# Kernel optimization log

Measured on AMD Instinct MI355X. Metric: run time of the kernel, lower is better.

## Reference

```python
import jax, jax.numpy as jnp
import numpy as np

DIM = 64
N_NEIGHBOR = 32
N_ENTITY = 1_000_000
N_RELATION = 64
N_USER = 500_000
BATCH = 16384


def _xavier_uniform(key, shape):
    fan_in, fan_out = shape[0], shape[1]
    bound = float(np.sqrt(6.0 / (fan_in + fan_out)))
    return jax.random.uniform(key, shape, jnp.float32, -bound, bound)


def setup_inputs() -> dict:
    key = jax.random.key(0)
    ks = jax.random.split(key, 10)
    users = jax.random.randint(ks[0], (BATCH,), 0, N_USER)
    items = jax.random.randint(ks[1], (BATCH,), 0, N_ENTITY)
    label = jnp.round(jax.random.uniform(ks[2], (BATCH,), jnp.float32))
    neighbor_rel = jax.random.randint(ks[3], (BATCH, N_NEIGHBOR), 0, N_RELATION)
    neighbor_tail = jax.random.randint(ks[4], (BATCH, N_NEIGHBOR), 0, N_ENTITY)
    user_emb = _xavier_uniform(ks[5], (N_USER, DIM))
    entity_emb = _xavier_uniform(ks[6], (N_ENTITY, DIM))
    relation_emb = _xavier_uniform(ks[7], (N_RELATION, DIM))
    in_dim = 2 * N_NEIGHBOR * DIM
    wb = float(np.sqrt(1.0 / in_dim))  # torch Linear default init bound
    gen_W = jax.random.uniform(ks[8], (DIM, in_dim), jnp.float32, -wb, wb)
    gen_b = jax.random.uniform(ks[9], (DIM,), jnp.float32, -wb, wb)
    return {"users": users, "items": items, "label": label,
            "neighbor_rel": neighbor_rel, "neighbor_tail": neighbor_tail,
            "user_emb": user_emb, "entity_emb": entity_emb,
            "relation_emb": relation_emb, "gen_W": gen_W, "gen_b": gen_b}


def _bce(p, y):
    # torch BCELoss: clamps log terms at -100, mean reduction
    logp = jnp.clip(jnp.log(p), -100.0)
    log1mp = jnp.clip(jnp.log1p(-p), -100.0)
    return -jnp.mean(y * logp + (1.0 - y) * log1mp)


def reference(users, items, label, neighbor_rel, neighbor_tail,
              user_emb, entity_emb, relation_emb, gen_W, gen_b):
    u = user_emb[users]                       # [B, D]
    i = entity_emb[items]                     # [B, D]
    predict = jax.nn.sigmoid(jnp.sum(u * i, axis=1))

    rel = relation_emb[neighbor_rel]          # [B, K, D]
    tail = entity_emb[neighbor_tail]          # [B, K, D]
    t_r = jnp.concatenate([rel, tail], axis=-1).reshape(u.shape[0], -1)  # [B, 2*K*D]
    false_item = jax.nn.sigmoid(t_r @ gen_W.T + gen_b)                   # [B, D]
    false_predict = jax.nn.sigmoid(jnp.sum(u * false_item, axis=1))

    return _bce(predict, label) + _bce(false_predict, label)
```

## Files before the change

kernel.cpp:

```cpp
#include <hip/hip_runtime.h>
#include <hip/hip_bf16.h>

#define BATCH 16384
#define DIM   64
#define NNB   32
#define INDIM 4096
#define BR    64
#define KC    128

typedef __attribute__((ext_vector_type(8))) short          s16x8;
typedef __attribute__((ext_vector_type(4))) float          f32x4;
typedef __attribute__((ext_vector_type(4))) unsigned int   u32x4;
typedef __attribute__((ext_vector_type(4))) unsigned short u16x4;

__device__ __forceinline__ float bf2f(unsigned short u) {
    union { unsigned int i; float f; } v;
    v.i = ((unsigned int)u) << 16;
    return v.f;
}

template<bool FP32>
__device__ __forceinline__ float ldT(const void* p, size_t i) {
    if constexpr (FP32) return ((const float*)p)[i];
    else                return bf2f(((const unsigned short*)p)[i]);
}

__global__ void kgnn_probe(const unsigned int* __restrict__ lab, int* __restrict__ flag) {
    if (threadIdx.x == 0) {
        int ok = 1;
        for (int i = 0; i < 32; ++i) {
            unsigned int w = lab[i];
            if (!(w == 0u || w == 0x3F800000u)) ok = 0;
        }
        *flag = ok;
    }
}

template<bool FP32>
__global__ __launch_bounds__(512, 2) void kgnn_mfma(
    const int* __restrict__ users, const int* __restrict__ items,
    const void* __restrict__ label_, const int* __restrict__ nrel,
    const int* __restrict__ ntail,  const void* __restrict__ uemb_,
    const void* __restrict__ eemb_, const void* __restrict__ remb_,
    const void* __restrict__ W_,    const void* __restrict__ b_,
    double* __restrict__ acc, const int* __restrict__ flag, const int force)
{
    if (force < 0 && *flag != (FP32 ? 1 : 0)) return;

    constexpr int TB = FP32 ? 32768 : 16384;
    constexpr int LO = 16384;
    __shared__ __align__(16) unsigned char ldsA[TB];
    __shared__ __align__(16) unsigned char ldsW[TB];
    __shared__ float p1s[BR];
    __shared__ float p2s[BR][2];

    const int t    = threadIdx.x;
    const int base = blockIdx.x * BR;
    const int lane = t & 63;
    const int w    = t >> 6;
    const int rt   = w & 3;
    const int dh   = w >> 2;
    const int r16  = lane & 15;
    const int kg   = lane >> 4;

    u32x4  rA16[2], rW16[2];
    float4 rA32[4], rW32[4];

    auto LOADS = [&](int n) {
        if constexpr (!FP32) {
            #pragma unroll
            for (int it = 0; it < 2; ++it) {
                const int lid = it * 512 + t;
                const int seg = lid >> 3, ln = lid & 7;
                const int row = seg >> 1, half = seg & 1;
                const int idx = half ? ntail[(size_t)(base + row) * NNB + n]
                                     : nrel [(size_t)(base + row) * NNB + n];
                const unsigned short* tbl = (const unsigned short*)(half ? eemb_ : remb_);
                rA16[it] = *(const u32x4*)(tbl + (size_t)idx * DIM + ln * 8);
            }
            #pragma unroll
            for (int it = 0; it < 2; ++it) {
                const int lid = it * 512 + t;
                const int d = lid >> 4, ln = lid & 15;
                rW16[it] = *(const u32x4*)((const unsigned short*)W_
                              + (size_t)d * INDIM + (size_t)n * KC + ln * 8);
            }
        } else {
            #pragma unroll
            for (int it = 0; it < 4; ++it) {
                const int lid = it * 512 + t;
                const int seg = lid >> 4, ln = lid & 15;
                const int row = seg >> 1, half = seg & 1;
                const int idx = half ? ntail[(size_t)(base + row) * NNB + n]
                                     : nrel [(size_t)(base + row) * NNB + n];
                const float* tbl = (const float*)(half ? eemb_ : remb_);
                rA32[it] = ((const float4*)(tbl + (size_t)idx * DIM))[ln];
            }
            #pragma unroll
            for (int it = 0; it < 4; ++it) {
                const int lid = it * 512 + t;
                const int d = lid >> 5, ln = lid & 31;
                rW32[it] = *(const float4*)((const float*)W_
                              + (size_t)d * INDIM + (size_t)n * KC + ln * 4);
            }
        }
    };

    auto split4 = [](const float4 v, u16x4& h, u16x4& l) {
        const float xs[4] = { v.x, v.y, v.z, v.w };
        #pragma unroll
        for (int j = 0; j < 4; ++j) {
            union { float f; unsigned u; } a, b, c;
            a.f = xs[j];
            const unsigned short hh = (unsigned short)(a.u >> 16);
            b.u = ((unsigned)hh) << 16;
            c.f = xs[j] - b.f;
            h[j] = hh;
            l[j] = (unsigned short)(c.u >> 16);
        }
    };

    auto WRITE = [&]() {
        if constexpr (!FP32) {
            #pragma unroll
            for (int it = 0; it < 2; ++it) {
                const int lid = it * 512 + t;
                const int seg = lid >> 3, ln = lid & 7;
                const int row = seg >> 1, half = seg & 1;
                const int byte = row * 256 + ((half * 128 + ln * 16) ^ ((row & 7) << 4));
                *(u32x4*)&ldsA[byte] = rA16[it];
            }
            #pragma unroll
            for (int it = 0; it < 2; ++it) {
                const int lid = it * 512 + t;
                const int d = lid >> 4, ln = lid & 15;
                const int byte = d * 256 + ((ln * 16) ^ ((d & 7) << 4));
                *(u32x4*)&ldsW[byte] = rW16[it];
            }
        } else {
            #pragma unroll
            for (int it = 0; it < 4; ++it) {
                const int lid = it * 512 + t;
                const int seg = lid >> 4, ln = lid & 15;
                const int row = seg >> 1, half = seg & 1;
                u16x4 h, l; split4(rA32[it], h, l);
                const int byte = row * 256 + ((half * 128 + ln * 8) ^ ((row & 7) << 4));
                *(u16x4*)&ldsA[byte]      = h;
                *(u16x4*)&ldsA[LO + byte] = l;
            }
            #pragma unroll
            for (int it = 0; it < 4; ++it) {
                const int lid = it * 512 + t;
                const int d = lid >> 5, ln = lid & 31;
                u16x4 h, l; split4(rW32[it], h, l);
                const int byte = d * 256 + ((ln * 8) ^ ((d & 7) << 4));
                *(u16x4*)&ldsW[byte]      = h;
                *(u16x4*)&ldsW[LO + byte] = l;
            }
        }
    };

    f32x4 acc0 = {0.f, 0.f, 0.f, 0.f};
    f32x4 acc1 = {0.f, 0.f, 0.f, 0.f};

    LOADS(0);
    WRITE();
    __syncthreads();

    for (int n = 0; n < NNB; ++n) {
        const bool more = (n + 1 < NNB);
        if (more) LOADS(n + 1);

        #pragma unroll
        for (int kk = 0; kk < 4; ++kk) {
            const int cb  = (kk * 64 + kg * 16) ^ ((r16 & 7) << 4);
            const int ra  = (rt * 16 + r16) * 256 + cb;
            const int rb0 = (dh * 32 + r16) * 256 + cb;
            const int rb1 = rb0 + 16 * 256;
            if constexpr (!FP32) {
                const s16x8 a  = *(const s16x8*)&ldsA[ra];
                const s16x8 b0 = *(const s16x8*)&ldsW[rb0];
                const s16x8 b1 = *(const s16x8*)&ldsW[rb1];
                acc0 = __builtin_amdgcn_mfma_f32_16x16x32_bf16(a, b0, acc0, 0, 0, 0);
                acc1 = __builtin_amdgcn_mfma_f32_16x16x32_bf16(a, b1, acc1, 0, 0, 0);
            } else {
                const s16x8 ah  = *(const s16x8*)&ldsA[ra];
                const s16x8 al  = *(const s16x8*)&ldsA[LO + ra];
                const s16x8 bh0 = *(const s16x8*)&ldsW[rb0];
                const s16x8 bl0 = *(const s16x8*)&ldsW[LO + rb0];
                const s16x8 bh1 = *(const s16x8*)&ldsW[rb1];
                const s16x8 bl1 = *(const s16x8*)&ldsW[LO + rb1];
                acc0 = __builtin_amdgcn_mfma_f32_16x16x32_bf16(ah, bh0, acc0, 0, 0, 0);
                acc0 = __builtin_amdgcn_mfma_f32_16x16x32_bf16(ah, bl0, acc0, 0, 0, 0);
                acc0 = __builtin_amdgcn_mfma_f32_16x16x32_bf16(al, bh0, acc0, 0, 0, 0);
                acc1 = __builtin_amdgcn_mfma_f32_16x16x32_bf16(ah, bh1, acc1, 0, 0, 0);
                acc1 = __builtin_amdgcn_mfma_f32_16x16x32_bf16(ah, bl1, acc1, 0, 0, 0);
                acc1 = __builtin_amdgcn_mfma_f32_16x16x32_bf16(al, bh1, acc1, 0, 0, 0);
            }
        }
        __syncthreads();
        if (more) WRITE();
        __syncthreads();
    }

    float part1[4] = {0.f, 0.f, 0.f, 0.f};
    float part2[4] = {0.f, 0.f, 0.f, 0.f};
    #pragma unroll
    for (int q = 0; q < 4; ++q) {
        const int r   = rt * 16 + kg * 4 + q;
        const int row = base + r;
        const int uid = users[row];
        #pragma unroll
        for (int j = 0; j < 2; ++j) {
            const int d  = (dh * 2 + j) * 16 + r16;
            const float fl = (j == 0 ? acc0[q] : acc1[q]) + ldT<FP32>(b_, d);
            const float fi = 1.f / (1.f + expf(-fl));
            const float uv = ldT<FP32>(uemb_, (size_t)uid * DIM + d);
            part2[q] += uv * fi;
        }
        if (dh == 0) {
            const int iid = items[row];
            #pragma unroll
            for (int jj = 0; jj < 4; ++jj) {
                const int d = jj * 16 + r16;
                const float uv = ldT<FP32>(uemb_, (size_t)uid * DIM + d);
                const float iv = ldT<FP32>(eemb_, (size_t)iid * DIM + d);
                part1[q] += uv * iv;
            }
        }
    }
    #pragma unroll
    for (int m = 1; m < 16; m <<= 1) {
        #pragma unroll
        for (int q = 0; q < 4; ++q) {
            part2[q] += __shfl_xor(part2[q], m, 64);
            part1[q] += __shfl_xor(part1[q], m, 64);
        }
    }
    if (r16 == 0) {
        #pragma unroll
        for (int q = 0; q < 4; ++q) {
            const int r = rt * 16 + kg * 4 + q;
            p2s[r][dh] = part2[q];
            if (dh == 0) p1s[r] = part1[q];
        }
    }
    __syncthreads();

    if (t < BR) {
        const int r = t, row = base + r;
        const float p1 = p1s[r];
        const float p2 = p2s[r][0] + p2s[r][1];
        const float y  = ldT<FP32>(label_, row);
        const float pa = 1.f / (1.f + expf(-p1));
        const float pb = 1.f / (1.f + expf(-p2));
        float term =
              y * fmaxf(logf(pa), -100.f) + (1.f - y) * fmaxf(log1pf(-pa), -100.f)
            + y * fmaxf(logf(pb), -100.f) + (1.f - y) * fmaxf(log1pf(-pb), -100.f);
        #pragma unroll
        for (int m = 1; m < 64; m <<= 1) term += __shfl_xor(term, m, 64);
        if (r == 0) atomicAdd(acc, (double)term);
    }
}

__global__ void kgnn_fin(const double* __restrict__ acc,
                         const int* __restrict__ flag, void* __restrict__ out,
                         const int mode) {
    if (threadIdx.x == 0 && blockIdx.x == 0) {
        const int m = (mode < 0) ? *flag : mode;
        const float loss = (float)(-(*acc) / (double)BATCH);
        if (m) ((float*)out)[0] = loss;
        else   ((__hip_bfloat16*)out)[0] = __float2bfloat16(loss);
    }
}

extern "C" void kernel_launch(void* const* d_in, const int* in_sizes, int n_in,
                              void* d_out, int out_size, void* d_ws, size_t ws_size,
                              hipStream_t stream) {
    const int* users = (const int*)d_in[0];
    const int* items = (const int*)d_in[1];
    const void* label = d_in[2];
    const int* nrel  = (const int*)d_in[3];
    const int* ntail = (const int*)d_in[4];
    const void* uemb = d_in[5];
    const void* eemb = d_in[6];
    const void* remb = d_in[7];
    const void* genW = d_in[8];
    const void* genb = d_in[9];

    double* acc = (double*)d_ws;
    int* flag   = (int*)((char*)d_ws + 8);
    hipMemsetAsync(d_ws, 0, 16, stream);

    const bool f32sz  = (out_size == 4) && (in_sizes[5] == 128000000);
    const bool bf16sz = (out_size == 2) && (in_sizes[5] == 64000000);
    const int grid = BATCH / BR;

    if (f32sz) {
        kgnn_mfma<true><<<grid, 512, 0, stream>>>(
            users, items, label, nrel, ntail, uemb, eemb, remb, genW, genb, acc, flag, 1);
        kgnn_fin<<<1, 64, 0, stream>>>(acc, flag, d_out, 1);
    } else if (bf16sz) {
        kgnn_mfma<false><<<grid, 512, 0, stream>>>(
            users, items, label, nrel, ntail, uemb, eemb, remb, genW, genb, acc, flag, 1);
        kgnn_fin<<<1, 64, 0, stream>>>(acc, flag, d_out, 0);
    } else {
        kgnn_probe<<<1, 64, 0, stream>>>((const unsigned int*)label, flag);
        kgnn_mfma<false><<<grid, 512, 0, stream>>>(
            users, items, label, nrel, ntail, uemb, eemb, remb, genW, genb, acc, flag, -1);
        kgnn_mfma<true><<<grid, 512, 0, stream>>>(
            users, items, label, nrel, ntail, uemb, eemb, remb, genW, genb, acc, flag, -1);
        kgnn_fin<<<1, 64, 0, stream>>>(acc, flag, d_out, -1);
    }
}
```

Baseline: 439.8 us.

## Rewrite gather-GEMM to load operands directly into registers with split-K waves

The kernel drops the LDS-staged, double-buffered A/W tiles. Each wave now gathers embedding rows and W slices straight from global memory into MFMA operands, with the neighbor indices cached in LDS. Block rows shrink from 64 to 32, the K dimension is split across two wave groups that are reduced through LDS, occupancy is raised to 4 blocks per CU, and the final reduction writes per-block partial sums instead of using double atomics. This removes the per-step barriers and LDS traffic. In exchange, W is re-read from global or L2 by every block with no LDS reuse, and the fp32 path recomputes the W hi/lo split in every block.

Result: slower. 522.0 us (+18.7%).

```diff
diff --git a/kernel.cpp b/kernel.cpp
--- a/kernel.cpp
+++ b/kernel.cpp
@@ -5,12 +5,11 @@
 #define DIM   64
 #define NNB   32
 #define INDIM 4096
-#define BR    64
-#define KC    128
+#define BR    32
+#define NBLK  (BATCH / BR)
 
 typedef __attribute__((ext_vector_type(8))) short          s16x8;
 typedef __attribute__((ext_vector_type(4))) float          f32x4;
-typedef __attribute__((ext_vector_type(4))) unsigned int   u32x4;
 typedef __attribute__((ext_vector_type(4))) unsigned short u16x4;
 
 __device__ __forceinline__ float bf2f(unsigned short u) {
@@ -23,6 +22,33 @@
 __device__ __forceinline__ float ldT(const void* p, size_t i) {
     if constexpr (FP32) return ((const float*)p)[i];
     else                return bf2f(((const unsigned short*)p)[i]);
+}
+
+template<bool FP32>
+__device__ __forceinline__ f32x4 ld4(const void* p, size_t i) {
+    if constexpr (FP32) {
+        return *(const f32x4*)((const float*)p + i);
+    } else {
+        const u16x4 v = *(const u16x4*)((const unsigned short*)p + i);
+        f32x4 r;
+        #pragma unroll
+        for (int j = 0; j < 4; ++j) r[j] = bf2f(v[j]);
+        return r;
+    }
+}
+
+__device__ __forceinline__ void split8(const f32x4 x, const f32x4 y, s16x8& h, s16x8& l) {
+    #pragma unroll
+    for (int j = 0; j < 8; ++j) {
+        const float v = (j < 4) ? x[j] : y[j - 4];
+        union { float f; unsigned u; } a, b, c;
+        a.f = v;
+        const unsigned short hh = (unsigned short)(a.u >> 16);
+        b.u = ((unsigned)hh) << 16;
+        c.f = v - b.f;
+        h[j] = (short)hh;
+        l[j] = (short)(c.u >> 16);
+    }
 }
 
 __global__ void kgnn_probe(const unsigned int* __restrict__ lab, int* __restrict__ flag) {
@@ -37,240 +63,173 @@
 }
 
 template<bool FP32>
-__global__ __launch_bounds__(512, 2) void kgnn_mfma(
+__global__ __launch_bounds__(512, 4) void kgnn_gemm(
     const int* __restrict__ users, const int* __restrict__ items,
     const void* __restrict__ label_, const int* __restrict__ nrel,
     const int* __restrict__ ntail,  const void* __restrict__ uemb_,
     const void* __restrict__ eemb_, const void* __restrict__ remb_,
     const void* __restrict__ W_,    const void* __restrict__ b_,
-    double* __restrict__ acc, const int* __restrict__ flag, const int force)
+    double* __restrict__ acc, double* __restrict__ bsum,
+    const int* __restrict__ flag, const int force)
 {
     if (force < 0 && *flag != (FP32 ? 1 : 0)) return;
 
-    constexpr int TB = FP32 ? 32768 : 16384;
-    constexpr int LO = 16384;
-    __shared__ __align__(16) unsigned char ldsA[TB];
-    __shared__ __align__(16) unsigned char ldsW[TB];
-    __shared__ float p1s[BR];
-    __shared__ float p2s[BR][2];
+    __shared__ int   sidx[2][BR][NNB + 1];
+    __shared__ float fl[2][BR][DIM];
+    __shared__ float st[BR];
 
     const int t    = threadIdx.x;
     const int base = blockIdx.x * BR;
     const int lane = t & 63;
     const int w    = t >> 6;
-    const int rt   = w & 3;
-    const int dh   = w >> 2;
     const int r16  = lane & 15;
     const int kg   = lane >> 4;
-
-    u32x4  rA16[2], rW16[2];
-    float4 rA32[4], rW32[4];
-
-    auto LOADS = [&](int n) {
-        if constexpr (!FP32) {
+    const int dt   = w & 3;
+    const int kh   = w >> 2;
+
+    #pragma unroll
+    for (int it = 0; it < 2; ++it) {
+        const int e = it * 512 + t;
+        const int row = e >> 5, n = e & 31;
+        sidx[0][row][n] = nrel [(size_t)base * NNB + e];
+        sidx[1][row][n] = ntail[(size_t)base * NNB + e];
+    }
+    __syncthreads();
+
+    f32x4 ac[2] = { {0.f,0.f,0.f,0.f}, {0.f,0.f,0.f,0.f} };
+    const int dcol = dt * 16 + r16;
+
+    if constexpr (!FP32) {
+        const unsigned short* E  = (const unsigned short*)eemb_;
+        const unsigned short* R  = (const unsigned short*)remb_;
+        const unsigned short* wb = (const unsigned short*)W_ + (size_t)dcol * INDIM + kg * 8;
+        #pragma unroll 2
+        for (int nn = 0; nn < NNB / 2; ++nn) {
+            const int n = kh * (NNB / 2) + nn;
+            const unsigned short* wn = wb + n * 128;
+            const s16x8 b0 = *(const s16x8*)(wn);
+            const s16x8 b1 = *(const s16x8*)(wn + 32);
+            const s16x8 b2 = *(const s16x8*)(wn + 64);
+            const s16x8 b3 = *(const s16x8*)(wn + 96);
             #pragma unroll
-            for (int it = 0; it < 2; ++it) {
-                const int lid = it * 512 + t;
-                const int seg = lid >> 3, ln = lid & 7;
-                const int row = seg >> 1, half = seg & 1;
-                const int idx = half ? ntail[(size_t)(base + row) * NNB + n]
-                                     : nrel [(size_t)(base + row) * NNB + n];
-                const unsigned short* tbl = (const unsigned short*)(half ? eemb_ : remb_);
-                rA16[it] = *(const u32x4*)(tbl + (size_t)idx * DIM + ln * 8);
+            for (int rt = 0; rt < 2; ++rt) {
+                const int ri = sidx[0][rt * 16 + r16][n];
+                const int ti = sidx[1][rt * 16 + r16][n];
+                const unsigned short* rr = R + (size_t)ri * DIM + kg * 8;
+                const unsigned short* tr = E + (size_t)ti * DIM + kg * 8;
+                const s16x8 a0 = *(const s16x8*)(rr);
+                const s16x8 a1 = *(const s16x8*)(rr + 32);
+                const s16x8 a2 = *(const s16x8*)(tr);
+                const s16x8 a3 = *(const s16x8*)(tr + 32);
+                ac[rt] = __builtin_amdgcn_mfma_f32_16x16x32_bf16(a0, b0, ac[rt], 0, 0, 0);
+                ac[rt] = __builtin_amdgcn_mfma_f32_16x16x32_bf16(a1, b1, ac[rt], 0, 0, 0);
+                ac[rt] = __builtin_amdgcn_mfma_f32_16x16x32_bf16(a2, b2, ac[rt], 0, 0, 0);
+                ac[rt] = __builtin_amdgcn_mfma_f32_16x16x32_bf16(a3, b3, ac[rt], 0, 0, 0);
             }
+        }
+    } else {
+        const float* E  = (const float*)eemb_;
+        const float* R  = (const float*)remb_;
+        const float* wb = (const float*)W_ + (size_t)dcol * INDIM + kg * 8;
+        for (int nn = 0; nn < NNB / 2; ++nn) {
+            const int n = kh * (NNB / 2) + nn;
+            const float* wn = wb + n * 128;
+            s16x8 bh[4], bl[4];
             #pragma unroll
-            for (int it = 0; it < 2; ++it) {
-                const int lid = it * 512 + t;
-                const int d = lid >> 4, ln = lid & 15;
-                rW16[it] = *(const u32x4*)((const unsigned short*)W_
-                              + (size_t)d * INDIM + (size_t)n * KC + ln * 8);
+            for (int s = 0; s < 4; ++s)
+                split8(*(const f32x4*)(wn + s * 32), *(const f32x4*)(wn + s * 32 + 4),
+                       bh[s], bl[s]);
+            #pragma unroll
+            for (int rt = 0; rt < 2; ++rt) {
+                const int ri = sidx[0][rt * 16 + r16][n];
+                const int ti = sidx[1][rt * 16 + r16][n];
+                const float* rr = R + (size_t)ri * DIM + kg * 8;
+                const float* tr = E + (size_t)ti * DIM + kg * 8;
+                #pragma unroll
+                for (int s = 0; s < 4; ++s) {
+                    const float* ap = (s < 2) ? rr + s * 32 : tr + (s - 2) * 32;
+                    s16x8 ah, al;
+                    split8(*(const f32x4*)(ap), *(const f32x4*)(ap + 4), ah, al);
+                    ac[rt] = __builtin_amdgcn_mfma_f32_16x16x32_bf16(ah, bh[s], ac[rt], 0, 0, 0);
+                    ac[rt] = __builtin_amdgcn_mfma_f32_16x16x32_bf16(ah, bl[s], ac[rt], 0, 0, 0);
+                    ac[rt] = __builtin_amdgcn_mfma_f32_16x16x32_bf16(al, bh[s], ac[rt], 0, 0, 0);
+                }
             }
-        } else {
-            #pragma unroll
-            for (int it = 0; it < 4; ++it) {
-                const int lid = it * 512 + t;
-                const int seg = lid >> 4, ln = lid & 15;
-                const int row = seg >> 1, half = seg & 1;
-                const int idx = half ? ntail[(size_t)(base + row) * NNB + n]
-                                     : nrel [(size_t)(base + row) * NNB + n];
-                const float* tbl = (const float*)(half ? eemb_ : remb_);
-                rA32[it] = ((const float4*)(tbl + (size_t)idx * DIM))[ln];
-            }
-            #pragma unroll
-            for (int it = 0; it < 4; ++it) {
-                const int lid = it * 512 + t;
-                const int d = lid >> 5, ln = lid & 31;
-                rW32[it] = *(const float4*)((const float*)W_
-                              + (size_t)d * INDIM + (size_t)n * KC + ln * 4);
-            }
-        }
-    };
-
-    auto split4 = [](const float4 v, u16x4& h, u16x4& l) {
-        const float xs[4] = { v.x, v.y, v.z, v.w };
+        }
+    }
+
+    #pragma unroll
+    for (int rt = 0; rt < 2; ++rt) {
+        #pragma unroll
+        for (int q = 0; q < 4; ++q)
+            fl[kh][rt * 16 + kg * 4 + q][dcol] = ac[rt][q];
+    }
+    __syncthreads();
+
+    {
+        const int row  = t >> 4;
+        const int c    = t & 15;
+        const int grow = base + row;
+        const int uid  = users[grow], iid = items[grow];
+        const f32x4 uv = ld4<FP32>(uemb_, (size_t)uid * DIM + c * 4);
+        const f32x4 iv = ld4<FP32>(eemb_, (size_t)iid * DIM + c * 4);
+        const f32x4 bv = ld4<FP32>(b_, (size_t)c * 4);
+        float p1 = 0.f, p2 = 0.f;
         #pragma unroll
         for (int j = 0; j < 4; ++j) {
-            union { float f; unsigned u; } a, b, c;
-            a.f = xs[j];
-            const unsigned short hh = (unsigned short)(a.u >> 16);
-            b.u = ((unsigned)hh) << 16;
-            c.f = xs[j] - b.f;
-            h[j] = hh;
-            l[j] = (unsigned short)(c.u >> 16);
-        }
-    };
-
-    auto WRITE = [&]() {
-        if constexpr (!FP32) {
-            #pragma unroll
-            for (int it = 0; it < 2; ++it) {
-                const int lid = it * 512 + t;
-                const int seg = lid >> 3, ln = lid & 7;
-                const int row = seg >> 1, half = seg & 1;
-                const int byte = row * 256 + ((half * 128 + ln * 16) ^ ((row & 7) << 4));
-                *(u32x4*)&ldsA[byte] = rA16[it];
-            }
-            #pragma unroll
-            for (int it = 0; it < 2; ++it) {
-                const int lid = it * 512 + t;
-                const int d = lid >> 4, ln = lid & 15;
-                const int byte = d * 256 + ((ln * 16) ^ ((d & 7) << 4));
-                *(u32x4*)&ldsW[byte] = rW16[it];
-            }
-        } else {
-            #pragma unroll
-            for (int it = 0; it < 4; ++it) {
-                const int lid = it * 512 + t;
-                const int seg = lid >> 4, ln = lid & 15;
-                const int row = seg >> 1, half = seg & 1;
-                u16x4 h, l; split4(rA32[it], h, l);
-                const int byte = row * 256 + ((half * 128 + ln * 8) ^ ((row & 7) << 4));
-                *(u16x4*)&ldsA[byte]      = h;
-                *(u16x4*)&ldsA[LO + byte] = l;
-            }
-            #pragma unroll
-            for (int it = 0; it < 4; ++it) {
-                const int lid = it * 512 + t;
-                const int d = lid >> 5, ln = lid & 31;
-                u16x4 h, l; split4(rW32[it], h, l);
-                const int byte = d * 256 + ((ln * 8) ^ ((d & 7) << 4));
-                *(u16x4*)&ldsW[byte]      = h;
-                *(u16x4*)&ldsW[LO + byte] = l;
-            }
-        }
-    };
-
-    f32x4 acc0 = {0.f, 0.f, 0.f, 0.f};
-    f32x4 acc1 = {0.f, 0.f, 0.f, 0.f};
-
-    LOADS(0);
-    WRITE();
-    __syncthreads();
-
-    for (int n = 0; n < NNB; ++n) {
-        const bool more = (n + 1 < NNB);
-        if (more) LOADS(n + 1);
-
-        #pragma unroll
-        for (int kk = 0; kk < 4; ++kk) {
-            const int cb  = (kk * 64 + kg * 16) ^ ((r16 & 7) << 4);
-            const int ra  = (rt * 16 + r16) * 256 + cb;
-            const int rb0 = (dh * 32 + r16) * 256 + cb;
-            const int rb1 = rb0 + 16 * 256;
-            if constexpr (!FP32) {
-                const s16x8 a  = *(const s16x8*)&ldsA[ra];
-                const s16x8 b0 = *(const s16x8*)&ldsW[rb0];
-                const s16x8 b1 = *(const s16x8*)&ldsW[rb1];
-                acc0 = __builtin_amdgcn_mfma_f32_16x16x32_bf16(a, b0, acc0, 0, 0, 0);
-                acc1 = __builtin_amdgcn_mfma_f32_16x16x32_bf16(a, b1, acc1, 0, 0, 0);
-            } else {
-                const s16x8 ah  = *(const s16x8*)&ldsA[ra];
-                const s16x8 al  = *(const s16x8*)&ldsA[LO + ra];
-                const s16x8 bh0 = *(const s16x8*)&ldsW[rb0];
-                const s16x8 bl0 = *(const s16x8*)&ldsW[LO + rb0];
-                const s16x8 bh1 = *(const s16x8*)&ldsW[rb1];
-                const s16x8 bl1 = *(const s16x8*)&ldsW[LO + rb1];
-                acc0 = __builtin_amdgcn_mfma_f32_16x16x32_bf16(ah, bh0, acc0, 0, 0, 0);
-                acc0 = __builtin_amdgcn_mfma_f32_16x16x32_bf16(ah, bl0, acc0, 0, 0, 0);
-                acc0 = __builtin_amdgcn_mfma_f32_16x16x32_bf16(al, bh0, acc0, 0, 0, 0);
-                acc1 = __builtin_amdgcn_mfma_f32_16x16x32_bf16(ah, bh1, acc1, 0, 0, 0);
-                acc1 = __builtin_amdgcn_mfma_f32_16x16x32_bf16(ah, bl1, acc1, 0, 0, 0);
-                acc1 = __builtin_amdgcn_mfma_f32_16x16x32_bf16(al, bh1, acc1, 0, 0, 0);
-            }
-        }
-        __syncthreads();
-        if (more) WRITE();
-        __syncthreads();
-    }
-
-    float part1[4] = {0.f, 0.f, 0.f, 0.f};
-    float part2[4] = {0.f, 0.f, 0.f, 0.f};
-    #pragma unroll
-    for (int q = 0; q < 4; ++q) {
-        const int r   = rt * 16 + kg * 4 + q;
-        const int row = base + r;
-        const int uid = users[row];
-        #pragma unroll
-        for (int j = 0; j < 2; ++j) {
-            const int d  = (dh * 2 + j) * 16 + r16;
-            const float fl = (j == 0 ? acc0[q] : acc1[q]) + ldT<FP32>(b_, d);
-            const float fi = 1.f / (1.f + expf(-fl));
-            const float uv = ldT<FP32>(uemb_, (size_t)uid * DIM + d);
-            part2[q] += uv * fi;
-        }
-        if (dh == 0) {
-            const int iid = items[row];
-            #pragma unroll
-            for (int jj = 0; jj < 4; ++jj) {
-                const int d = jj * 16 + r16;
-                const float uv = ldT<FP32>(uemb_, (size_t)uid * DIM + d);
-                const float iv = ldT<FP32>(eemb_, (size_t)iid * DIM + d);
-                part1[q] += uv * iv;
-            }
-        }
-    }
-    #pragma unroll
-    for (int m = 1; m < 16; m <<= 1) {
-        #pragma unroll
-        for (int q = 0; q < 4; ++q) {
-            part2[q] += __shfl_xor(part2[q], m, 64);
-            part1[q] += __shfl_xor(part1[q], m, 64);
-        }
-    }
-    if (r16 == 0) {
-        #pragma unroll
-        for (int q = 0; q < 4; ++q) {
-            const int r = rt * 16 + kg * 4 + q;
-            p2s[r][dh] = part2[q];
-            if (dh == 0) p1s[r] = part1[q];
-        }
-    }
-    __syncthreads();
-
-    if (t < BR) {
-        const int r = t, row = base + r;
-        const float p1 = p1s[r];
-        const float p2 = p2s[r][0] + p2s[r][1];
-        const float y  = ldT<FP32>(label_, row);
-        const float pa = 1.f / (1.f + expf(-p1));
-        const float pb = 1.f / (1.f + expf(-p2));
-        float term =
-              y * fmaxf(logf(pa), -100.f) + (1.f - y) * fmaxf(log1pf(-pa), -100.f)
-            + y * fmaxf(logf(pb), -100.f) + (1.f - y) * fmaxf(log1pf(-pb), -100.f);
-        #pragma unroll
-        for (int m = 1; m < 64; m <<= 1) term += __shfl_xor(term, m, 64);
-        if (r == 0) atomicAdd(acc, (double)term);
-    }
-}
-
-__global__ void kgnn_fin(const double* __restrict__ acc,
+            const float lg = fl[0][row][c * 4 + j] + fl[1][row][c * 4 + j] + bv[j];
+            const float fi = 1.f / (1.f + expf(-lg));
+            p2 += uv[j] * fi;
+            p1 += uv[j] * iv[j];
+        }
+        #pragma unroll
+        for (int m = 1; m < 16; m <<= 1) {
+            p1 += __shfl_xor(p1, m, 16);
+            p2 += __shfl_xor(p2, m, 16);
+        }
+        if (c == 0) {
+            const float y  = ldT<FP32>(label_, grow);
+            const float pa = 1.f / (1.f + expf(-p1));
+            const float pb = 1.f / (1.f + expf(-p2));
+            st[row] =
+                  y * fmaxf(logf(pa), -100.f) + (1.f - y) * fmaxf(log1pf(-pa), -100.f)
+                + y * fmaxf(logf(pb), -100.f) + (1.f - y) * fmaxf(log1pf(-pb), -100.f);
+        }
+    }
+    __syncthreads();
+
+    if (t < 64) {
+        float s = (t < BR) ? st[t] : 0.f;
+        #pragma unroll
+        for (int m = 1; m < 64; m <<= 1) s += __shfl_xor(s, m, 64);
+        if (t == 0) {
+            if (bsum) bsum[blockIdx.x] = (double)s;
+            else      atomicAdd(acc, (double)s);
+        }
+    }
+}
+
+__global__ void kgnn_fin(const double* __restrict__ acc, const double* __restrict__ bsum,
                          const int* __restrict__ flag, void* __restrict__ out,
                          const int mode) {
-    if (threadIdx.x == 0 && blockIdx.x == 0) {
-        const int m = (mode < 0) ? *flag : mode;
-        const float loss = (float)(-(*acc) / (double)BATCH);
-        if (m) ((float*)out)[0] = loss;
-        else   ((__hip_bfloat16*)out)[0] = __float2bfloat16(loss);
+    __shared__ double sd[4];
+    const int t = threadIdx.x;
+    double s = 0.0;
+    if (bsum) {
+        for (int i = t; i < NBLK; i += 256) s += bsum[i];
+    } else if (t == 0) {
+        s = *acc;
+    }
+    #pragma unroll
+    for (int m = 1; m < 64; m <<= 1) s += __shfl_xor(s, m, 64);
+    if ((t & 63) == 0) sd[t >> 6] = s;
+    __syncthreads();
+    if (t == 0) {
+        const double tot = sd[0] + sd[1] + sd[2] + sd[3];
+        const int md = (mode < 0) ? *flag : mode;
+        const float loss = (float)(-tot / (double)BATCH);
+        if (md) ((float*)out)[0] = loss;
+        else    ((__hip_bfloat16*)out)[0] = __float2bfloat16(loss);
     }
 }
 
@@ -288,28 +247,33 @@
     const void* genW = d_in[8];
     const void* genb = d_in[9];
 
-    double* acc = (double*)d_ws;
-    int* flag   = (int*)((char*)d_ws + 8);
+    double* acc  = (double*)d_ws;
+    int*    flag = (int*)((char*)d_ws + 8);
+    double* bsum = (ws_size >= (size_t)(16 + NBLK * 8))
+                       ? (double*)((char*)d_ws + 16) : nullptr;
     hipMemsetAsync(d_ws, 0, 16, stream);
 
     const bool f32sz  = (out_size == 4) && (in_sizes[5] == 128000000);
     const bool bf16sz = (out_size == 2) && (in_sizes[5] == 64000000);
-    const int grid = BATCH / BR;
 
     if (f32sz) {
-        kgnn_mfma<true><<<grid, 512, 0, stream>>>(
-            users, items, label, nrel, ntail, uemb, eemb, remb, genW, genb, acc, flag, 1);
-        kgnn_fin<<<1, 64, 0, stream>>>(acc, flag, d_out, 1);
+        kgnn_gemm<true><<<NBLK, 512, 0, stream>>>(
+            users, items, label, nrel, ntail, uemb, eemb, remb, genW, genb,
+            acc, bsum, flag, 1);
+        kgnn_fin<<<1, 256, 0, stream>>>(acc, bsum, flag, d_out, 1);
     } else if (bf16sz) {
-        kgnn_mfma<false><<<grid, 512, 0, stream>>>(
-            users, items, label, nrel, ntail, uemb, eemb, remb, genW, genb, acc, flag, 1);
-        kgnn_fin<<<1, 64, 0, stream>>>(acc, flag, d_out, 0);
+        kgnn_gemm<false><<<NBLK, 512, 0, stream>>>(
+            users, items, label, nrel, ntail, uemb, eemb, remb, genW, genb,
+            acc, bsum, flag, 0);
+        kgnn_fin<<<1, 256, 0, stream>>>(acc, bsum, flag, d_out, 0);
     } else {
         kgnn_probe<<<1, 64, 0, stream>>>((const unsigned int*)label, flag);
-        kgnn_mfma<false><<<grid, 512, 0, stream>>>(
-            users, items, label, nrel, ntail, uemb, eemb, remb, genW, genb, acc, flag, -1);
-        kgnn_mfma<true><<<grid, 512, 0, stream>>>(
-            users, items, label, nrel, ntail, uemb, eemb, remb, genW, genb, acc, flag, -1);
-        kgnn_fin<<<1, 64, 0, stream>>>(acc, flag, d_out, -1);
-    }
-}
+        kgnn_gemm<false><<<NBLK, 512, 0, stream>>>(
+            users, items, label, nrel, ntail, uemb, eemb, remb, genW, genb,
+            acc, bsum, flag, -1);
+        kgnn_gemm<true><<<NBLK, 512, 0, stream>>>(
+            users, items, label, nrel, ntail, uemb, eemb, remb, genW, genb,
+            acc, bsum, flag, -1);
+        kgnn_fin<<<1, 256, 0, stream>>>(acc, bsum, flag, d_out, -1);
+    }
+}
```
